# Kernel optimization log

Hardware: AMD Instinct MI355X
Metric: run time of the kernel (lower is better)

## Reference

```python
import jax, jax.numpy as jnp
import numpy as np

D_MODEL = 1024
N_HEADS = 16
HEAD_DIM = D_MODEL // N_HEADS


def setup_inputs() -> dict:
    key = jax.random.key(0)
    ks = jax.random.split(key, 11)
    B, S = 4, 2048
    scale = 1.0 / np.sqrt(D_MODEL)
    inp = {
        "Q": jax.random.normal(ks[0], (B, S, D_MODEL), jnp.float32),
        "K": jax.random.normal(ks[1], (B, S, D_MODEL), jnp.float32),
        "V": jax.random.normal(ks[2], (B, S, D_MODEL), jnp.float32),
        "Wq": jax.random.normal(ks[3], (D_MODEL, D_MODEL), jnp.float32) * scale,
        "bq": jnp.zeros((D_MODEL,), jnp.float32),
        "Wk": jax.random.normal(ks[4], (D_MODEL, D_MODEL), jnp.float32) * scale,
        "bk": jnp.zeros((D_MODEL,), jnp.float32),
        "Wv": jax.random.normal(ks[5], (D_MODEL, D_MODEL), jnp.float32) * scale,
        "bv": jnp.zeros((D_MODEL,), jnp.float32),
        "Wo": jax.random.normal(ks[6], (D_MODEL, D_MODEL), jnp.float32) * scale,
        "bo": jnp.zeros((D_MODEL,), jnp.float32),
    }
    return inp


def reference(Q, K, V, Wq, bq, Wk, bk, Wv, bv, Wo, bo):
    B, S, _ = Q.shape
    # Linear projections (torch nn.Linear: x @ W.T + b)
    q = Q @ Wq.T + bq
    k = K @ Wk.T + bk
    v = V @ Wv.T + bv
    # [B, S, H, Dh] -> [B, H, S, Dh]
    q = q.reshape(B, S, N_HEADS, HEAD_DIM).transpose(0, 2, 1, 3)
    k = k.reshape(B, S, N_HEADS, HEAD_DIM).transpose(0, 2, 1, 3)
    v = v.reshape(B, S, N_HEADS, HEAD_DIM).transpose(0, 2, 1, 3)
    inv_sqrt_dh = 1.0 / np.sqrt(HEAD_DIM)
    scores = jnp.einsum("bhqd,bhkd->bhqk", q, k) * inv_sqrt_dh  # [B,H,S,S]
    attn = jax.nn.softmax(scores, axis=-1)
    out = jnp.einsum("bhqk,bhkd->bhqd", attn, v)  # [B,H,S,Dh]
    out = out.transpose(0, 2, 1, 3).reshape(B, S, D_MODEL)
    return out @ Wo.T + bo
```

## Files before the change

### kernel.cpp

```cpp
#include <hip/hip_runtime.h>
#include <hip/hip_bf16.h>
#include <stdint.h>
#include <stddef.h>


typedef __bf16 bf16_t;
typedef __bf16 bf16x4 __attribute__((ext_vector_type(4)));
typedef __bf16 bf16x8 __attribute__((ext_vector_type(8)));
typedef float f32x4 __attribute__((ext_vector_type(4)));

#define D_MODEL 1024
#define M_ROWS  8192
#define S_LEN   2048
#define N_HEADS 16
#define HEAD_DIM 64
#define GBK 32
#define NT (D_MODEL / GBK)

__device__ __forceinline__ void async_copy16(void* lds, const void* g) {
    __builtin_amdgcn_global_load_lds(
        (const __attribute__((address_space(1))) void*)g,
        (__attribute__((address_space(3))) void*)lds, 16, 0, 0);
}

__device__ __forceinline__ uint32_t cvt_pk_bf16(float lo, float hi) {
    uint32_t r;
    asm("v_cvt_pk_bf16_f32 %0, %1, %2" : "=v"(r) : "v"(lo), "v"(hi));
    return r;
}

__global__ __launch_bounds__(256) void conv_w(
    const float* __restrict__ s0, const float* __restrict__ s1, const float* __restrict__ s2,
    bf16_t* __restrict__ d0, bf16_t* __restrict__ d1, bf16_t* __restrict__ d2)
{
    const float* s; bf16_t* d;
    if (blockIdx.y == 0)      { s = s0; d = d0; }
    else if (blockIdx.y == 1) { s = s1; d = d1; }
    else                      { s = s2; d = d2; }
    const int i = (blockIdx.x * 256 + threadIdx.x) * 8;
    const f32x4 a = *(const f32x4*)(s + i);
    const f32x4 b = *(const f32x4*)(s + i + 4);
    bf16x8 o;
#pragma unroll
    for (int j = 0; j < 4; j++) { o[j] = (bf16_t)a[j]; o[4 + j] = (bf16_t)b[j]; }
    *(bf16x8*)(d + i) = o;
}

__global__ __launch_bounds__(256, 3) void gemm_proj(
    const float* __restrict__ A0, const bf16_t* __restrict__ W0, const float* __restrict__ b0,
    const float* __restrict__ A1, const bf16_t* __restrict__ W1, const float* __restrict__ b1,
    const float* __restrict__ A2, const bf16_t* __restrict__ W2, const float* __restrict__ b2,
    bf16_t* C0, bf16_t* C1, bf16_t* C2)
{
    const int lin = blockIdx.x + ((int)blockIdx.y << 3) + ((int)blockIdx.z << 9);
    const int nl  = (lin & 7) * 192 + (lin >> 3);
    const int z   = nl >> 9;
    const int rem = nl & 511;
    const int bm0 = (rem >> 3) * 128;
    const int bn0 = (rem & 7) * 128;

    const float* A; const bf16_t* W; const float* bias; bf16_t* C;
    if (z == 0)      { A = A0; W = W0; bias = b0; C = C0; }
    else if (z == 1) { A = A1; W = W1; bias = b1; C = C1; }
    else             { A = A2; W = W2; bias = b2; C = C2; }
    const float cs = (z == 0) ? 0.125f : (z == 1) ? 1.4426950408889634f : 1.0f;

    __align__(16) __shared__ bf16_t sA[2][128 * 36];
    __align__(16) __shared__ bf16_t sW[2][128 * GBK];

    const int t    = threadIdx.x;
    const int lane = t & 63;
    const int w    = t >> 6;
    const int wm   = (w & 1) * 64;
    const int wn   = (w >> 1) * 64;
    const int q4   = lane >> 4;
    const int l16  = lane & 15;

    const int srow  = t >> 1;
    const int cbase = (t & 1) * 2;
    const float* aptr = &A[(size_t)(bm0 + srow) * D_MODEL + cbase * 8];

    auto stageW = [&](int buf, int kt) {
#pragma unroll
        for (int i = 0; i < 2; i++) {
            const int cid = i * 256 + t;
            const int row = cid >> 2;
            const int cg  = (cid & 3) ^ ((row >> 1) & 3);
            async_copy16(&sW[buf][cid * 8],
                         &W[(size_t)(bn0 + row) * D_MODEL + kt * GBK + cg * 8]);
        }
    };
    auto writeA = [&](int buf, f32x4 (&ar)[4]) {
        bf16x8 abf[2];
#pragma unroll
        for (int c = 0; c < 4; c++)
#pragma unroll
            for (int j = 0; j < 4; j++)
                abf[c >> 1][(c & 1) * 4 + j] = (bf16_t)ar[c][j];
#pragma unroll
        for (int hb = 0; hb < 2; hb++) {
            const int slot = (cbase + hb) ^ (srow & 3);
            *(bf16x8*)&sA[buf][srow * 36 + slot * 8] = abf[hb];
        }
    };

    stageW(0, 0);
    f32x4 arA[4], arB[4];
#pragma unroll
    for (int c = 0; c < 4; c++) arA[c] = *(const f32x4*)(aptr + c * 4);
#pragma unroll
    for (int c = 0; c < 4; c++) arB[c] = *(const f32x4*)(aptr + GBK + c * 4);
    writeA(0, arA);
    asm volatile("s_waitcnt vmcnt(4) lgkmcnt(0)" ::: "memory");
    __builtin_amdgcn_s_barrier();
    __builtin_amdgcn_sched_barrier(0);

    f32x4 acc[4][4];
    const f32x4 zero4 = {0.f, 0.f, 0.f, 0.f};
#pragma unroll
    for (int i = 0; i < 4; i++)
#pragma unroll
        for (int j = 0; j < 4; j++) acc[i][j] = zero4;

    auto body = [&](int kt, int buf, f32x4 (&arCur)[4], f32x4 (&arNext)[4]) {
        if (kt + 1 < NT) stageW(buf ^ 1, kt + 1);
        if (kt + 2 < NT) {
            const float* ap = aptr + (size_t)(kt + 2) * GBK;
#pragma unroll
            for (int c = 0; c < 4; c++) arNext[c] = *(const f32x4*)(ap + c * 4);
        }

        bf16x8 af[4], bfr[4];
#pragma unroll
        for (int i = 0; i < 4; i++) {
            const int m = wm + i * 16 + l16;
            af[i]  = *(const bf16x8*)&sA[buf][m * 36 + (q4 ^ (m & 3)) * 8];
            const int n = wn + i * 16 + l16;
            bfr[i] = *(const bf16x8*)&sW[buf][n * GBK + (q4 ^ ((n >> 1) & 3)) * 8];
        }
#pragma unroll
        for (int i = 0; i < 4; i++)
#pragma unroll
            for (int j = 0; j < 4; j++)
                acc[i][j] = __builtin_amdgcn_mfma_f32_16x16x32_bf16(af[i], bfr[j], acc[i][j], 0, 0, 0);

        __builtin_amdgcn_sched_barrier(0);
        if (kt + 1 < NT) writeA(buf ^ 1, arCur);
        if (kt + 2 < NT) asm volatile("s_waitcnt vmcnt(4) lgkmcnt(0)" ::: "memory");
        else             asm volatile("s_waitcnt vmcnt(0) lgkmcnt(0)" ::: "memory");
        __builtin_amdgcn_s_barrier();
        __builtin_amdgcn_sched_barrier(0);
    };

    for (int kt = 0; kt < NT; kt += 2) {
        body(kt,     0, arB, arA);
        body(kt + 1, 1, arA, arB);
    }

    if (z != 2) {
#pragma unroll
        for (int j = 0; j < 4; j++) {
            const int col = bn0 + wn + j * 16 + l16;
            const float bj = bias[col];
#pragma unroll
            for (int i = 0; i < 4; i++) {
                const int rowb = bm0 + wm + i * 16 + q4 * 4;
#pragma unroll
                for (int r = 0; r < 4; r++)
                    C[(size_t)(rowb + r) * D_MODEL + col] = (bf16_t)((acc[i][j][r] + bj) * cs);
            }
        }
    } else {
        const int bb = bm0 >> 11;
        const int sbase = (bm0 & 2047) + wm;
#pragma unroll
        for (int j = 0; j < 4; j++) {
            const int col = bn0 + wn + j * 16 + l16;
            const float bj = bias[col];
            bf16_t* ct = C + ((size_t)bb * 1024 + col) * 2048;
#pragma unroll
            for (int i = 0; i < 4; i++) {
                const int s0 = sbase + i * 16 + q4 * 4;
                const int s0p = (s0 & ~31) | (((s0 >> 2) & 3) << 3) | (((s0 >> 4) & 1) << 2);
                bf16x4 v4;
#pragma unroll
                for (int r = 0; r < 4; r++) v4[r] = (bf16_t)(acc[i][j][r] + bj);
                *(bf16x4*)&ct[s0p] = v4;
            }
        }
    }
}

__global__ __launch_bounds__(256, 3) void gemm_out(
    const bf16_t* __restrict__ A, const bf16_t* __restrict__ W,
    const float* __restrict__ bias, float* __restrict__ C)
{
    const int lin = blockIdx.x + ((int)blockIdx.y << 3);
    const int nl  = (lin & 7) * 64 + (lin >> 3);
    const int bm0 = (nl >> 3) * 128;
    const int bn0 = (nl & 7) * 128;

    __align__(16) __shared__ bf16_t sA[2][128 * GBK];
    __align__(16) __shared__ bf16_t sW[2][128 * GBK];

    const int t    = threadIdx.x;
    const int lane = t & 63;
    const int w    = t >> 6;
    const int wm   = (w & 1) * 64;
    const int wn   = (w >> 1) * 64;
    const int q4   = lane >> 4;
    const int l16  = lane & 15;

    auto stage = [&](int buf, int kt) {
#pragma unroll
        for (int i = 0; i < 2; i++) {
            const int cid = i * 256 + t;
            const int row = cid >> 2;
            const int cg  = (cid & 3) ^ ((row >> 1) & 3);
            async_copy16(&sA[buf][cid * 8],
                         &A[(size_t)(bm0 + row) * D_MODEL + kt * GBK + cg * 8]);
            async_copy16(&sW[buf][cid * 8],
                         &W[(size_t)(bn0 + row) * D_MODEL + kt * GBK + cg * 8]);
        }
    };

    stage(0, 0);

    f32x4 acc[4][4];
    const f32x4 zero4 = {0.f, 0.f, 0.f, 0.f};
#pragma unroll
    for (int i = 0; i < 4; i++)
#pragma unroll
        for (int j = 0; j < 4; j++) acc[i][j] = zero4;

    for (int kt = 0; kt < NT; ++kt) {
        const int buf = kt & 1;
        __syncthreads();
        if (kt + 1 < NT) stage(buf ^ 1, kt + 1);

        bf16x8 af[4], bfr[4];
#pragma unroll
        for (int i = 0; i < 4; i++) {
            const int m = wm + i * 16 + l16;
            af[i]  = *(const bf16x8*)&sA[buf][m * GBK + (q4 ^ ((m >> 1) & 3)) * 8];
            const int n = wn + i * 16 + l16;
            bfr[i] = *(const bf16x8*)&sW[buf][n * GBK + (q4 ^ ((n >> 1) & 3)) * 8];
        }
#pragma unroll
        for (int i = 0; i < 4; i++)
#pragma unroll
            for (int j = 0; j < 4; j++)
                acc[i][j] = __builtin_amdgcn_mfma_f32_16x16x32_bf16(af[i], bfr[j], acc[i][j], 0, 0, 0);
    }

#pragma unroll
    for (int j = 0; j < 4; j++) {
        const int col = bn0 + wn + j * 16 + l16;
        const float bj = bias[col];
#pragma unroll
        for (int i = 0; i < 4; i++) {
            const int rowb = bm0 + wm + i * 16 + q4 * 4;
#pragma unroll
            for (int r = 0; r < 4; r++)
                C[(size_t)(rowb + r) * D_MODEL + col] = acc[i][j][r] + bj;
        }
    }
}

#define KVT (S_LEN / 128)

__global__ __launch_bounds__(512, 3) void attn_fused(
    const bf16_t* __restrict__ q, const bf16_t* __restrict__ k,
    const bf16_t* __restrict__ vt, bf16_t* o)
{
    __align__(16) __shared__ bf16_t sK[2][128 * 64];
    __align__(16) __shared__ bf16_t sVt[2][64 * 128];

    const int t    = threadIdx.x;
    const int lane = t & 63;
    const int w    = t >> 6;
    const int head = blockIdx.x;
    const int b    = head >> 4;
    const int h    = head & 15;
    const size_t base = (size_t)b * S_LEN * D_MODEL + (size_t)h * HEAD_DIM;
    const bf16_t* vth = vt + ((size_t)b * 1024 + h * 64) * 2048;
    const int qt0  = blockIdx.y * 256;
    const int q4   = lane >> 4;
    const int l16  = lane & 15;

    bf16x8 qf[2][2];
#pragma unroll
    for (int mg = 0; mg < 2; mg++)
#pragma unroll
        for (int kk = 0; kk < 2; kk++)
            qf[mg][kk] = *(const bf16x8*)&q[base + (size_t)(qt0 + w * 32 + mg * 16 + l16) * D_MODEL + kk * 32 + q4 * 8];

    const f32x4 zero4 = {0.f, 0.f, 0.f, 0.f};
    f32x4 oacc[2][4];
#pragma unroll
    for (int mg = 0; mg < 2; mg++)
#pragma unroll
        for (int g = 0; g < 4; g++) oacc[mg][g] = zero4;
    f32x4 sacc[2] = {zero4, zero4};

    bf16x8 ones;
#pragma unroll
    for (int j = 0; j < 8; j++) ones[j] = (bf16_t)1.0f;

    auto stage = [&](int bf, int kt) {
        const int key0 = kt * 128;
#pragma unroll
        for (int i = 0; i < 2; i++) {
            const int cid = i * 512 + t;
            const int row = cid >> 3;
            const int cg  = (cid & 7) ^ (row & 7);
            async_copy16(&sK[bf][cid * 8], &k[base + (size_t)(key0 + row) * D_MODEL + cg * 8]);
        }
#pragma unroll
        for (int i = 0; i < 2; i++) {
            const int cid = i * 512 + t;
            const int dh  = cid >> 4;
            const int cg  = (cid & 15) ^ (dh & 15);
            async_copy16(&sVt[bf][cid * 8], &vth[(size_t)dh * 2048 + key0 + cg * 8]);
        }
    };

    stage(0, 0);
    asm volatile("s_waitcnt vmcnt(0)" ::: "memory");
    __builtin_amdgcn_s_barrier();
    __builtin_amdgcn_sched_barrier(0);

    for (int kt = 0; kt < KVT; ++kt) {
        const int cur = kt & 1;
        if (kt < KVT - 1) stage(cur ^ 1, kt + 1);

#pragma unroll
        for (int hh = 0; hh < 2; hh++) {
            f32x4 sc[2][4];
            __builtin_amdgcn_s_setprio(1);
#pragma unroll
            for (int ngl = 0; ngl < 4; ngl++) {
                const int key = (hh * 4 + ngl) * 16 + l16;
                const bf16x8 kf0 = *(const bf16x8*)&sK[cur][key * 64 + ((q4) ^ (key & 7)) * 8];
                const bf16x8 kf1 = *(const bf16x8*)&sK[cur][key * 64 + ((4 + q4) ^ (key & 7)) * 8];
#pragma unroll
                for (int mg = 0; mg < 2; mg++) {
                    sc[mg][ngl] = __builtin_amdgcn_mfma_f32_16x16x32_bf16(kf0, qf[mg][0], zero4, 0, 0, 0);
                    sc[mg][ngl] = __builtin_amdgcn_mfma_f32_16x16x32_bf16(kf1, qf[mg][1], sc[mg][ngl], 0, 0, 0);
                }
            }
            __builtin_amdgcn_s_setprio(0);

            bf16x8 pf[2][2];
#pragma unroll
            for (int mg = 0; mg < 2; mg++) {
#pragma unroll
                for (int ngl = 0; ngl < 4; ngl++)
#pragma unroll
                    for (int r = 0; r < 4; r++)
                        sc[mg][ngl][r] = exp2f(sc[mg][ngl][r]);
#pragma unroll
                for (int cl = 0; cl < 2; cl++) {
                    union { uint32_t u[4]; bf16x8 v; } pk;
#pragma unroll
                    for (int dw = 0; dw < 4; dw++) {
                        const int c = cl * 2 + (dw >> 1);
                        const int e = (dw & 1) * 2;
                        pk.u[dw] = cvt_pk_bf16(sc[mg][c][e], sc[mg][c][e + 1]);
                    }
                    pf[mg][cl] = pk.v;
                }
            }

            __builtin_amdgcn_s_setprio(1);
#pragma unroll
            for (int cl = 0; cl < 2; cl++) {
                const int cb = (hh * 2 + cl) * 4;
#pragma unroll
                for (int g = 0; g < 4; g++) {
                    const int dh = g * 16 + l16;
                    const bf16x8 vf = *(const bf16x8*)&sVt[cur][dh * 128 + ((cb + q4) ^ l16) * 8];
#pragma unroll
                    for (int mg = 0; mg < 2; mg++)
                        oacc[mg][g] = __builtin_amdgcn_mfma_f32_16x16x32_bf16(pf[mg][cl], vf, oacc[mg][g], 0, 0, 0);
                }
#pragma unroll
                for (int mg = 0; mg < 2; mg++)
                    sacc[mg] = __builtin_amdgcn_mfma_f32_16x16x32_bf16(pf[mg][cl], ones, sacc[mg], 0, 0, 0);
            }
            __builtin_amdgcn_s_setprio(0);
        }

        asm volatile("s_waitcnt vmcnt(0)" ::: "memory");
        __builtin_amdgcn_s_barrier();
        __builtin_amdgcn_sched_barrier(0);
    }

#pragma unroll
    for (int mg = 0; mg < 2; mg++)
#pragma unroll
        for (int r = 0; r < 4; r++) {
            const float inv = 1.0f / sacc[mg][r];
            const size_t rowoff = base + (size_t)(qt0 + w * 32 + mg * 16 + q4 * 4 + r) * D_MODEL;
#pragma unroll
            for (int g = 0; g < 4; g++)
                o[rowoff + g * 16 + l16] = (bf16_t)(oacc[mg][g][r] * inv);
        }
}

extern "C" void kernel_launch(void* const* d_in, const int* in_sizes, int n_in,
                              void* d_out, int out_size, void* d_ws, size_t ws_size,
                              hipStream_t stream) {
    const float* Q  = (const float*)d_in[0];
    const float* K  = (const float*)d_in[1];
    const float* V  = (const float*)d_in[2];
    const float* Wq = (const float*)d_in[3];
    const float* bq = (const float*)d_in[4];
    const float* Wk = (const float*)d_in[5];
    const float* bk = (const float*)d_in[6];
    const float* Wv = (const float*)d_in[7];
    const float* bv = (const float*)d_in[8];
    const float* Wo = (const float*)d_in[9];
    const float* bo = (const float*)d_in[10];
    float* out = (float*)d_out;

    bf16_t* qb  = (bf16_t*)d_ws;
    bf16_t* vb  = qb + (size_t)M_ROWS * D_MODEL;
    bf16_t* kb  = (bf16_t*)d_out;
    bf16_t* wqb = kb + (size_t)M_ROWS * D_MODEL;
    bf16_t* wkb = wqb + (size_t)D_MODEL * D_MODEL;
    bf16_t* wvb = wkb + (size_t)D_MODEL * D_MODEL;
    bf16_t* wob = vb;
    bf16_t* ob  = qb;

    conv_w<<<dim3(512, 3), dim3(256), 0, stream>>>(Wq, Wk, Wv, wqb, wkb, wvb);
    gemm_proj<<<dim3(8, 64, 3), dim3(256), 0, stream>>>(Q, wqb, bq, K, wkb, bk, V, wvb, bv, qb, kb, vb);
    attn_fused<<<dim3(4 * N_HEADS, S_LEN / 256), dim3(512), 0, stream>>>(qb, kb, vb, ob);
    conv_w<<<dim3(512, 1), dim3(256), 0, stream>>>(Wo, Wo, Wo, wob, wob, wob);
    gemm_out<<<dim3(8, 64), dim3(256), 0, stream>>>(ob, wob, bo, out);
}
```

Before: 358.3 us.

## Enlarge projection and output GEMM tiles to 128x256 with BK=64 and 512 threads

Both the QKV-projection and output-projection GEMMs move from 128x128 tiles with K-step 32 and 256 threads to 128x256 tiles with K-step 64 and 512 threads (8 waves), on a flattened 1-D grid with a new block-swizzle mapping. In the projection GEMM, the fp32 activation tile is now staged straight into LDS with async global-to-LDS copies, and is converted to bf16 with packed cvt when fragments are read. This replaces the earlier register-staged load, convert and LDS write. The goal is more reuse per loaded byte and half as many barriers per K sweep. In exchange, the projection kernel uses about 128KB of LDS per block, which limits occupancy, and each iteration waits on vmcnt(0), which may expose load latency.

```diff
diff --git a/kernel.cpp b/kernel.cpp
--- a/kernel.cpp
+++ b/kernel.cpp
@@ -14,8 +14,8 @@
 #define S_LEN   2048
 #define N_HEADS 16
 #define HEAD_DIM 64
-#define GBK 32
-#define NT (D_MODEL / GBK)
+#define BK2 64
+#define KT2 (D_MODEL / BK2)
 
 __device__ __forceinline__ void async_copy16(void* lds, const void* g) {
     __builtin_amdgcn_global_load_lds(
@@ -46,18 +46,18 @@
     *(bf16x8*)(d + i) = o;
 }
 
-__global__ __launch_bounds__(256, 3) void gemm_proj(
+__global__ __launch_bounds__(512, 2) void gemm_proj(
     const float* __restrict__ A0, const bf16_t* __restrict__ W0, const float* __restrict__ b0,
     const float* __restrict__ A1, const bf16_t* __restrict__ W1, const float* __restrict__ b1,
     const float* __restrict__ A2, const bf16_t* __restrict__ W2, const float* __restrict__ b2,
     bf16_t* C0, bf16_t* C1, bf16_t* C2)
 {
-    const int lin = blockIdx.x + ((int)blockIdx.y << 3) + ((int)blockIdx.z << 9);
-    const int nl  = (lin & 7) * 192 + (lin >> 3);
-    const int z   = nl >> 9;
-    const int rem = nl & 511;
-    const int bm0 = (rem >> 3) * 128;
-    const int bn0 = (rem & 7) * 128;
+    const int lin = blockIdx.x;
+    const int nl  = (lin & 7) * 96 + (lin >> 3);
+    const int z   = nl >> 8;
+    const int rem = nl & 255;
+    const int bm0 = (rem >> 2) * 128;
+    const int bn0 = (rem & 3) * 256;
 
     const float* A; const bf16_t* W; const float* bias; bf16_t* C;
     if (z == 0)      { A = A0; W = W0; bias = b0; C = C0; }
@@ -65,8 +65,8 @@
     else             { A = A2; W = W2; bias = b2; C = C2; }
     const float cs = (z == 0) ? 0.125f : (z == 1) ? 1.4426950408889634f : 1.0f;
 
-    __align__(16) __shared__ bf16_t sA[2][128 * 36];
-    __align__(16) __shared__ bf16_t sW[2][128 * GBK];
+    __align__(16) __shared__ float  sAf[2][128 * BK2];
+    __align__(16) __shared__ bf16_t sB[2][256 * BK2];
 
     const int t    = threadIdx.x;
     const int lane = t & 63;
@@ -76,42 +76,27 @@
     const int q4   = lane >> 4;
     const int l16  = lane & 15;
 
-    const int srow  = t >> 1;
-    const int cbase = (t & 1) * 2;
-    const float* aptr = &A[(size_t)(bm0 + srow) * D_MODEL + cbase * 8];
-
-    auto stageW = [&](int buf, int kt) {
-#pragma unroll
-        for (int i = 0; i < 2; i++) {
-            const int cid = i * 256 + t;
-            const int row = cid >> 2;
-            const int cg  = (cid & 3) ^ ((row >> 1) & 3);
-            async_copy16(&sW[buf][cid * 8],
-                         &W[(size_t)(bn0 + row) * D_MODEL + kt * GBK + cg * 8]);
+    auto stage = [&](int buf, int kt) {
+#pragma unroll
+        for (int i = 0; i < 4; i++) {
+            const int cid = i * 512 + t;
+            {
+                const int row = cid >> 4;
+                const int cg  = (cid & 15) ^ (row & 15);
+                async_copy16(&sAf[buf][cid * 4],
+                             &A[(size_t)(bm0 + row) * D_MODEL + kt * BK2 + cg * 4]);
+            }
+            {
+                const int row = cid >> 3;
+                const int cg  = (cid & 7) ^ (row & 7);
+                async_copy16(&sB[buf][cid * 8],
+                             &W[(size_t)(bn0 + row) * D_MODEL + kt * BK2 + cg * 8]);
+            }
         }
     };
-    auto writeA = [&](int buf, f32x4 (&ar)[4]) {
-        bf16x8 abf[2];
-#pragma unroll
-        for (int c = 0; c < 4; c++)
-#pragma unroll
-            for (int j = 0; j < 4; j++)
-                abf[c >> 1][(c & 1) * 4 + j] = (bf16_t)ar[c][j];
-#pragma unroll
-        for (int hb = 0; hb < 2; hb++) {
-            const int slot = (cbase + hb) ^ (srow & 3);
-            *(bf16x8*)&sA[buf][srow * 36 + slot * 8] = abf[hb];
-        }
-    };
-
-    stageW(0, 0);
-    f32x4 arA[4], arB[4];
-#pragma unroll
-    for (int c = 0; c < 4; c++) arA[c] = *(const f32x4*)(aptr + c * 4);
-#pragma unroll
-    for (int c = 0; c < 4; c++) arB[c] = *(const f32x4*)(aptr + GBK + c * 4);
-    writeA(0, arA);
-    asm volatile("s_waitcnt vmcnt(4) lgkmcnt(0)" ::: "memory");
+
+    stage(0, 0);
+    asm volatile("s_waitcnt vmcnt(0)" ::: "memory");
     __builtin_amdgcn_s_barrier();
     __builtin_amdgcn_sched_barrier(0);
 
@@ -122,39 +107,48 @@
 #pragma unroll
         for (int j = 0; j < 4; j++) acc[i][j] = zero4;
 
-    auto body = [&](int kt, int buf, f32x4 (&arCur)[4], f32x4 (&arNext)[4]) {
-        if (kt + 1 < NT) stageW(buf ^ 1, kt + 1);
-        if (kt + 2 < NT) {
-            const float* ap = aptr + (size_t)(kt + 2) * GBK;
-#pragma unroll
-            for (int c = 0; c < 4; c++) arNext[c] = *(const f32x4*)(ap + c * 4);
-        }
-
-        bf16x8 af[4], bfr[4];
+    for (int kt = 0; kt < KT2; ++kt) {
+        const int buf = kt & 1;
+        if (kt + 1 < KT2) stage(buf ^ 1, kt + 1);
+
+        bf16x8 af[4][2];
 #pragma unroll
         for (int i = 0; i < 4; i++) {
-            const int m = wm + i * 16 + l16;
-            af[i]  = *(const bf16x8*)&sA[buf][m * 36 + (q4 ^ (m & 3)) * 8];
-            const int n = wn + i * 16 + l16;
-            bfr[i] = *(const bf16x8*)&sW[buf][n * GBK + (q4 ^ ((n >> 1) & 3)) * 8];
-        }
-#pragma unroll
-        for (int i = 0; i < 4; i++)
-#pragma unroll
-            for (int j = 0; j < 4; j++)
-                acc[i][j] = __builtin_amdgcn_mfma_f32_16x16x32_bf16(af[i], bfr[j], acc[i][j], 0, 0, 0);
-
-        __builtin_amdgcn_sched_barrier(0);
-        if (kt + 1 < NT) writeA(buf ^ 1, arCur);
-        if (kt + 2 < NT) asm volatile("s_waitcnt vmcnt(4) lgkmcnt(0)" ::: "memory");
-        else             asm volatile("s_waitcnt vmcnt(0) lgkmcnt(0)" ::: "memory");
+            const int row = wm + i * 16 + l16;
+#pragma unroll
+            for (int kk = 0; kk < 2; kk++) {
+                const int c0 = kk * 8 + q4 * 2;
+                const f32x4 lo = *(const f32x4*)&sAf[buf][row * BK2 + ((c0    ) ^ (row & 15)) * 4];
+                const f32x4 hi = *(const f32x4*)&sAf[buf][row * BK2 + ((c0 + 1) ^ (row & 15)) * 4];
+                union { uint32_t u[4]; bf16x8 v; } pk;
+                pk.u[0] = cvt_pk_bf16(lo[0], lo[1]);
+                pk.u[1] = cvt_pk_bf16(lo[2], lo[3]);
+                pk.u[2] = cvt_pk_bf16(hi[0], hi[1]);
+                pk.u[3] = cvt_pk_bf16(hi[2], hi[3]);
+                af[i][kk] = pk.v;
+            }
+        }
+        bf16x8 bfr[4][2];
+#pragma unroll
+        for (int j = 0; j < 4; j++) {
+            const int row = wn + j * 16 + l16;
+#pragma unroll
+            for (int kk = 0; kk < 2; kk++) {
+                const int c = kk * 4 + q4;
+                bfr[j][kk] = *(const bf16x8*)&sB[buf][row * BK2 + (c ^ (row & 7)) * 8];
+            }
+        }
+#pragma unroll
+        for (int kk = 0; kk < 2; kk++)
+#pragma unroll
+            for (int i = 0; i < 4; i++)
+#pragma unroll
+                for (int j = 0; j < 4; j++)
+                    acc[i][j] = __builtin_amdgcn_mfma_f32_16x16x32_bf16(af[i][kk], bfr[j][kk], acc[i][j], 0, 0, 0);
+
+        asm volatile("s_waitcnt vmcnt(0) lgkmcnt(0)" ::: "memory");
         __builtin_amdgcn_s_barrier();
         __builtin_amdgcn_sched_barrier(0);
-    };
-
-    for (int kt = 0; kt < NT; kt += 2) {
-        body(kt,     0, arB, arA);
-        body(kt + 1, 1, arA, arB);
     }
 
     if (z != 2) {
@@ -191,17 +185,17 @@
     }
 }
 
-__global__ __launch_bounds__(256, 3) void gemm_out(
+__global__ __launch_bounds__(512, 2) void gemm_out(
     const bf16_t* __restrict__ A, const bf16_t* __restrict__ W,
     const float* __restrict__ bias, float* __restrict__ C)
 {
-    const int lin = blockIdx.x + ((int)blockIdx.y << 3);
-    const int nl  = (lin & 7) * 64 + (lin >> 3);
-    const int bm0 = (nl >> 3) * 128;
-    const int bn0 = (nl & 7) * 128;
-
-    __align__(16) __shared__ bf16_t sA[2][128 * GBK];
-    __align__(16) __shared__ bf16_t sW[2][128 * GBK];
+    const int lin = blockIdx.x;
+    const int nl  = (lin & 7) * 32 + (lin >> 3);
+    const int bm0 = (nl >> 2) * 128;
+    const int bn0 = (nl & 3) * 256;
+
+    __align__(16) __shared__ bf16_t sAo[2][128 * BK2];
+    __align__(16) __shared__ bf16_t sB[2][256 * BK2];
 
     const int t    = threadIdx.x;
     const int lane = t & 63;
@@ -214,17 +208,26 @@
     auto stage = [&](int buf, int kt) {
 #pragma unroll
         for (int i = 0; i < 2; i++) {
-            const int cid = i * 256 + t;
-            const int row = cid >> 2;
-            const int cg  = (cid & 3) ^ ((row >> 1) & 3);
-            async_copy16(&sA[buf][cid * 8],
-                         &A[(size_t)(bm0 + row) * D_MODEL + kt * GBK + cg * 8]);
-            async_copy16(&sW[buf][cid * 8],
-                         &W[(size_t)(bn0 + row) * D_MODEL + kt * GBK + cg * 8]);
+            const int cid = i * 512 + t;
+            const int row = cid >> 3;
+            const int cg  = (cid & 7) ^ (row & 7);
+            async_copy16(&sAo[buf][cid * 8],
+                         &A[(size_t)(bm0 + row) * D_MODEL + kt * BK2 + cg * 8]);
+        }
+#pragma unroll
+        for (int i = 0; i < 4; i++) {
+            const int cid = i * 512 + t;
+            const int row = cid >> 3;
+            const int cg  = (cid & 7) ^ (row & 7);
+            async_copy16(&sB[buf][cid * 8],
+                         &W[(size_t)(bn0 + row) * D_MODEL + kt * BK2 + cg * 8]);
         }
     };
 
     stage(0, 0);
+    asm volatile("s_waitcnt vmcnt(0)" ::: "memory");
+    __builtin_amdgcn_s_barrier();
+    __builtin_amdgcn_sched_barrier(0);
 
     f32x4 acc[4][4];
     const f32x4 zero4 = {0.f, 0.f, 0.f, 0.f};
@@ -233,24 +236,36 @@
 #pragma unroll
         for (int j = 0; j < 4; j++) acc[i][j] = zero4;
 
-    for (int kt = 0; kt < NT; ++kt) {
+    for (int kt = 0; kt < KT2; ++kt) {
         const int buf = kt & 1;
-        __syncthreads();
-        if (kt + 1 < NT) stage(buf ^ 1, kt + 1);
-
-        bf16x8 af[4], bfr[4];
+        if (kt + 1 < KT2) stage(buf ^ 1, kt + 1);
+
+        bf16x8 af[4][2], bfr[4][2];
 #pragma unroll
         for (int i = 0; i < 4; i++) {
-            const int m = wm + i * 16 + l16;
-            af[i]  = *(const bf16x8*)&sA[buf][m * GBK + (q4 ^ ((m >> 1) & 3)) * 8];
-            const int n = wn + i * 16 + l16;
-            bfr[i] = *(const bf16x8*)&sW[buf][n * GBK + (q4 ^ ((n >> 1) & 3)) * 8];
-        }
-#pragma unroll
-        for (int i = 0; i < 4; i++)
-#pragma unroll
-            for (int j = 0; j < 4; j++)
-                acc[i][j] = __builtin_amdgcn_mfma_f32_16x16x32_bf16(af[i], bfr[j], acc[i][j], 0, 0, 0);
+            const int row = wm + i * 16 + l16;
+#pragma unroll
+            for (int kk = 0; kk < 2; kk++)
+                af[i][kk] = *(const bf16x8*)&sAo[buf][row * BK2 + ((kk * 4 + q4) ^ (row & 7)) * 8];
+        }
+#pragma unroll
+        for (int j = 0; j < 4; j++) {
+            const int row = wn + j * 16 + l16;
+#pragma unroll
+            for (int kk = 0; kk < 2; kk++)
+                bfr[j][kk] = *(const bf16x8*)&sB[buf][row * BK2 + ((kk * 4 + q4) ^ (row & 7)) * 8];
+        }
+#pragma unroll
+        for (int kk = 0; kk < 2; kk++)
+#pragma unroll
+            for (int i = 0; i < 4; i++)
+#pragma unroll
+                for (int j = 0; j < 4; j++)
+                    acc[i][j] = __builtin_amdgcn_mfma_f32_16x16x32_bf16(af[i][kk], bfr[j][kk], acc[i][j], 0, 0, 0);
+
+        asm volatile("s_waitcnt vmcnt(0) lgkmcnt(0)" ::: "memory");
+        __builtin_amdgcn_s_barrier();
+        __builtin_amdgcn_sched_barrier(0);
     }
 
 #pragma unroll
@@ -434,8 +449,8 @@
     bf16_t* ob  = qb;
 
     conv_w<<<dim3(512, 3), dim3(256), 0, stream>>>(Wq, Wk, Wv, wqb, wkb, wvb);
-    gemm_proj<<<dim3(8, 64, 3), dim3(256), 0, stream>>>(Q, wqb, bq, K, wkb, bk, V, wvb, bv, qb, kb, vb);
+    gemm_proj<<<dim3(768), dim3(512), 0, stream>>>(Q, wqb, bq, K, wkb, bk, V, wvb, bv, qb, kb, vb);
     attn_fused<<<dim3(4 * N_HEADS, S_LEN / 256), dim3(512), 0, stream>>>(qb, kb, vb, ob);
     conv_w<<<dim3(512, 1), dim3(256), 0, stream>>>(Wo, Wo, Wo, wob, wob, wob);
-    gemm_out<<<dim3(8, 64), dim3(256), 0, stream>>>(ob, wob, bo, out);
-}
+    gemm_out<<<dim3(256), dim3(512), 0, stream>>>(ob, wob, bo, out);
+}
```

Measured after the change: 369.4 us. +3.1%, slower.
